# Performance work log

Measured on AMD Instinct MI355X. Metric: run time of the kernel, lower is better.

## Reference

```python
import jax, jax.numpy as jnp
import numpy as np

N = 20000
NEG_SLOPE = 0.2


def gat_conv(x, src, dst, W, att_src, att_dst, bias, heads, ch, concat):
    # x: [N, F_in]; src/dst: [E] (messages flow src -> dst, softmax grouped by dst)
    n = x.shape[0]
    h = (x @ W).reshape(n, heads, ch)                      # [N, H, C]
    a_s = jnp.sum(h * att_src, axis=-1)                    # [N, H]
    a_d = jnp.sum(h * att_dst, axis=-1)                    # [N, H]
    e = jax.nn.leaky_relu(a_s[src] + a_d[dst], NEG_SLOPE)  # [E, H]
    m = jax.ops.segment_max(e, dst, num_segments=n)        # segment-softmax (stable)
    ex = jnp.exp(e - m[dst])
    denom = jax.ops.segment_sum(ex, dst, num_segments=n)
    alpha = ex / (denom[dst] + 1e-16)                      # [E, H]
    msg = h[src] * alpha[:, :, None]                       # [E, H, C]
    out = jax.ops.segment_sum(msg, dst, num_segments=n)    # [N, H, C]
    out = out.reshape(n, heads * ch) if concat else out.mean(axis=1)
    return out + bias


def setup_inputs() -> dict:
    key = jax.random.key(0)
    ks = jax.random.split(key, 24)
    in_ch, h_ch, out_ch, H, OH = 512, 128, 64, 4, 6
    hid = H * h_ch  # 512
    s = 0.1
    d = {
        "x": jax.random.normal(ks[0], (N, in_ch), jnp.float32),
        "edge_index": jax.random.randint(ks[1], (2, 160000), 0, N, jnp.int32),
        "W1": jax.random.normal(ks[2], (in_ch, H * h_ch), jnp.float32) * s,
        "as1": jax.random.normal(ks[3], (1, H, h_ch), jnp.float32) * s,
        "ad1": jax.random.normal(ks[4], (1, H, h_ch), jnp.float32) * s,
        "b1": jnp.zeros((H * h_ch,), jnp.float32),
        "lW1": jax.random.normal(ks[5], (in_ch, hid), jnp.float32) * s,
        "lb1": jnp.zeros((hid,), jnp.float32),
        "W2": jax.random.normal(ks[6], (hid, H * h_ch), jnp.float32) * s,
        "as2": jax.random.normal(ks[7], (1, H, h_ch), jnp.float32) * s,
        "ad2": jax.random.normal(ks[8], (1, H, h_ch), jnp.float32) * s,
        "b2": jnp.zeros((H * h_ch,), jnp.float32),
        "lW2": jax.random.normal(ks[9], (hid, hid), jnp.float32) * s,
        "lb2": jnp.zeros((hid,), jnp.float32),
        "W3": jax.random.normal(ks[10], (hid, OH * out_ch), jnp.float32) * s,
        "as3": jax.random.normal(ks[11], (1, OH, out_ch), jnp.float32) * s,
        "ad3": jax.random.normal(ks[12], (1, OH, out_ch), jnp.float32) * s,
        "b3": jnp.zeros((out_ch,), jnp.float32),
        "lW3": jax.random.normal(ks[13], (hid, out_ch), jnp.float32) * s,
        "lb3": jnp.zeros((out_ch,), jnp.float32),
    }
    return d


def reference(x, edge_index, W1, as1, ad1, b1, lW1, lb1,
              W2, as2, ad2, b2, lW2, lb2,
              W3, as3, ad3, b3, lW3, lb3):
    n = x.shape[0]
    loops = jnp.arange(n, dtype=edge_index.dtype)  # PyG GATConv add_self_loops=True
    src = jnp.concatenate([edge_index[0], loops])
    dst = jnp.concatenate([edge_index[1], loops])
    h = jax.nn.elu(gat_conv(x, src, dst, W1, as1, ad1, b1, 4, 128, True) + x @ lW1 + lb1)
    h = jax.nn.elu(gat_conv(h, src, dst, W2, as2, ad2, b2, 4, 128, True) + h @ lW2 + lb2)
    out = gat_conv(h, src, dst, W3, as3, ad3, b3, 6, 64, False) + h @ lW3 + lb3
    return out
```

## Files before the change

### kernel.cpp

```cpp
#include <hip/hip_runtime.h>
#include <cstddef>
#include <cstdint>
#include <type_traits>

#define N_NODES 20000
#define NPAD 20096
#define E0_EDGES 160000
#define E_TOT (E0_EDGES + N_NODES)
#define CAP 64

typedef __bf16 bf16x8 __attribute__((ext_vector_type(8)));
typedef float f32x4 __attribute__((ext_vector_type(4)));

__device__ __forceinline__ ushort f2bf(float f) {
  uint32_t u = __float_as_uint(f);
  return (ushort)((u + 0x7FFFu + ((u >> 16) & 1u)) >> 16);
}
__device__ __forceinline__ float bf2f(ushort h) {
  return __uint_as_float((uint32_t)h << 16);
}

__device__ __forceinline__ int SW(int r) { return ((r >> 1) & 3) ^ ((r >> 3) & 1); }

#define GLOAD16(g, l)                                                         \
  __builtin_amdgcn_global_load_lds(                                           \
      (const __attribute__((address_space(1))) void*)(uintptr_t)(g),          \
      (__attribute__((address_space(3))) void*)(uint32_t)(uintptr_t)(l),      \
      16, 0, 0)


__global__ void fill_csr_kernel(const int* __restrict__ ei, int* __restrict__ cnt,
                                int* __restrict__ slots) {
  int e = blockIdx.x * blockDim.x + threadIdx.x;
  if (e >= E_TOT) return;
  int src, dst;
  if (e < E0_EDGES) { src = ei[e]; dst = ei[E0_EDGES + e]; }
  else              { src = e - E0_EDGES; dst = src; }
  int pos = atomicAdd(&cnt[dst], 1);
  if (pos < CAP) slots[dst * CAP + pos] = src;
}


__global__ void convert_x_kernel(const float* __restrict__ x, ushort* __restrict__ xb) {
  size_t i = ((size_t)blockIdx.x * blockDim.x + threadIdx.x) * 4;
  if (i >= (size_t)NPAD * 512) return;
  if (i < (size_t)N_NODES * 512) {
    float4 v = *(const float4*)(x + i);
    ushort4 o;
    o.x = f2bf(v.x); o.y = f2bf(v.y); o.z = f2bf(v.z); o.w = f2bf(v.w);
    *(ushort4*)(xb + i) = o;
  } else {
    *(ushort4*)(xb + i) = make_ushort4(0, 0, 0, 0);
  }
}

__global__ void transpose_all_kernel(
    const float* __restrict__ W1, const float* __restrict__ lW1,
    const float* __restrict__ W2, const float* __restrict__ lW2,
    const float* __restrict__ W3, const float* __restrict__ lW3,
    ushort* __restrict__ Bt1, ushort* __restrict__ Bt2, ushort* __restrict__ Bt3) {
  __shared__ float tile[32][33];
  const int K = 512;
  int z = blockIdx.z;
  const float* W; ushort* B; int M;
  switch (z) {
    case 0:  W = W1;  B = Bt1;              M = 512; break;
    case 1:  W = lW1; B = Bt1 + 512 * 512;  M = 512; break;
    case 2:  W = W2;  B = Bt2;              M = 512; break;
    case 3:  W = lW2; B = Bt2 + 512 * 512;  M = 512; break;
    case 4:  W = W3;  B = Bt3;              M = 384; break;
    default: W = lW3; B = Bt3 + 384 * 512;  M = 64;  break;
  }
  int mb = blockIdx.x * 32, kb = blockIdx.y * 32;
  if (mb >= M) return;
  int tx = threadIdx.x, ty = threadIdx.y;
#pragma unroll
  for (int i = 0; i < 32; i += 8)
    tile[ty + i][tx] = W[(size_t)(kb + ty + i) * M + mb + tx];
  __syncthreads();
#pragma unroll
  for (int i = 0; i < 32; i += 8)
    B[(size_t)(mb + ty + i) * K + kb + tx] = f2bf(tile[tx][ty + i]);
}


template <typename Out1T>
__global__ __launch_bounds__(256, 2) void mfma_gemm_kernel(
    const ushort* __restrict__ A,
    const ushort* __restrict__ Bt,
    ushort* __restrict__ out0, int ld0, int split,
    Out1T* __restrict__ out1, int ld1, int Mout1, const float* __restrict__ bias1,
    const float* __restrict__ att_sw, const float* __restrict__ att_dw,
    float* __restrict__ a_sp, float* __restrict__ a_dp,
    int nheads, int headC,
    int NT, int nwg) {
  const int K = 512;
  __shared__ __attribute__((aligned(16))) ushort As[5][128][32];
  __shared__ __attribute__((aligned(16))) ushort Bs[5][128][32];

  int q = nwg >> 3, r = nwg & 7;
  int orig = blockIdx.x;
  int xcd = orig & 7, pos = orig >> 3;
  int wgid = (xcd < r ? xcd * (q + 1) : r * (q + 1) + (xcd - r) * q) + pos;
  int by = wgid / NT, bx = wgid - by * NT;
  int bm = by * 128, bn = bx * 128;

  int tid = threadIdx.x, lane = tid & 63, wave = tid >> 6;
  int wrow = (wave >> 1) * 64, wcol = (wave & 1) * 64;

  size_t K2 = (size_t)K * 2;
  int rofs = lane >> 2;
  int gch = (lane & 3) ^ SW(rofs);
  const char* pA[2];
  const char* pB[2];
  int srow[2];
#pragma unroll
  for (int it = 0; it < 2; ++it) {
    int rr = wave * 32 + it * 16 + rofs;
    srow[it] = wave * 32 + it * 16;
    pA[it] = (const char*)A + (size_t)(bm + rr) * K2 + gch * 16;
    pB[it] = (const char*)Bt + (size_t)(bn + rr) * K2 + gch * 16;
  }

  int fr = lane & 15, hi = lane >> 4;
  int rch = hi ^ SW(fr);

  f32x4 acc[4][4] = {};

  char* AsB = (char*)&As[0][0][0];
  char* BsB = (char*)&Bs[0][0][0];

#pragma unroll
  for (int s = 0; s < 4; ++s) {
#pragma unroll
    for (int it = 0; it < 2; ++it) {
      GLOAD16(pA[it], AsB + s * 8192 + srow[it] * 64);
      GLOAD16(pB[it], BsB + s * 8192 + srow[it] * 64);
    }
#pragma unroll
    for (int it = 0; it < 2; ++it) { pA[it] += 64; pB[it] += 64; }
  }

#pragma unroll
  for (int k = 0; k < 16; ++k) {
    if (k < 13)       asm volatile("s_waitcnt vmcnt(12) lgkmcnt(0)" ::: "memory");
    else if (k == 13) asm volatile("s_waitcnt vmcnt(8) lgkmcnt(0)"  ::: "memory");
    else if (k == 14) asm volatile("s_waitcnt vmcnt(4) lgkmcnt(0)"  ::: "memory");
    else              asm volatile("s_waitcnt vmcnt(0) lgkmcnt(0)"  ::: "memory");
    __builtin_amdgcn_s_barrier();
    asm volatile("" ::: "memory");
    if (k + 4 < 16) {
      int ss = (k + 4) % 5;
#pragma unroll
      for (int it = 0; it < 2; ++it) {
        GLOAD16(pA[it], AsB + ss * 8192 + srow[it] * 64);
        GLOAD16(pB[it], BsB + ss * 8192 + srow[it] * 64);
      }
#pragma unroll
      for (int it = 0; it < 2; ++it) { pA[it] += 64; pB[it] += 64; }
    }
    {
      int sc = k % 5;
      bf16x8 af[4], bf[4];
#pragma unroll
      for (int i = 0; i < 4; ++i)
        af[i] = *(const bf16x8*)&As[sc][wrow + i * 16 + fr][rch * 8];
#pragma unroll
      for (int j = 0; j < 4; ++j)
        bf[j] = *(const bf16x8*)&Bs[sc][wcol + j * 16 + fr][rch * 8];
#pragma unroll
      for (int i = 0; i < 4; ++i)
#pragma unroll
        for (int j = 0; j < 4; ++j)
          acc[i][j] = __builtin_amdgcn_mfma_f32_16x16x32_bf16(af[i], bf[j], acc[i][j], 0, 0, 0);
    }
    asm volatile("" ::: "memory");
  }

  int colg = bn + wcol;
  bool lower = colg < split;
  int g4 = hi << 2;
  int ccol = fr;
#pragma unroll
  for (int i = 0; i < 4; ++i) {
#pragma unroll
    for (int rr = 0; rr < 4; ++rr) {
      int row = bm + wrow + g4 + i * 16 + rr;
      if (row >= N_NODES) continue;
#pragma unroll
      for (int j = 0; j < 4; ++j) {
        int col = colg + j * 16 + ccol;
        float v = acc[i][j][rr];
        if (lower) {
          out0[(size_t)row * ld0 + col] = f2bf(v);
        } else {
          int c1 = col - split;
          if (c1 < Mout1) {
            float b = v + bias1[c1];
            if constexpr (std::is_same<Out1T, ushort>::value)
              out1[(size_t)row * ld1 + c1] = f2bf(b);
            else
              out1[(size_t)row * ld1 + c1] = b;
          }
        }
      }
    }
  }

  if (lower) {
    int hd = colg / headC;
    int cb = colg - hd * headC;
    int half = (cb >> 6) & 1;
    float ws4[4], wd4[4];
#pragma unroll
    for (int j = 0; j < 4; ++j) {
      int cc = hd * headC + cb + j * 16 + ccol;
      ws4[j] = att_sw[cc];
      wd4[j] = att_dw[cc];
    }
#pragma unroll
    for (int i = 0; i < 4; ++i) {
#pragma unroll
      for (int rr = 0; rr < 4; ++rr) {
        float ps = 0.f, pd = 0.f;
#pragma unroll
        for (int j = 0; j < 4; ++j) { ps += acc[i][j][rr] * ws4[j]; pd += acc[i][j][rr] * wd4[j]; }
#pragma unroll
        for (int o = 1; o < 16; o <<= 1) { ps += __shfl_xor(ps, o); pd += __shfl_xor(pd, o); }
        if ((lane & 15) == 0) {
          int row = bm + wrow + g4 + i * 16 + rr;
          if (row < N_NODES) {
            size_t idx = ((size_t)row * nheads + hd) * 2;
            if (headC == 128) {
              a_sp[idx + half] = ps;
              a_dp[idx + half] = pd;
            } else {
              a_sp[idx] = ps;  a_sp[idx + 1] = 0.f;
              a_dp[idx] = pd;  a_dp[idx + 1] = 0.f;
            }
          }
        }
      }
    }
  }
}


template <int H, int C>
__global__ __launch_bounds__(128) void gather12_fused(
    const int* __restrict__ cnt, const int* __restrict__ slots,
    const float* __restrict__ a_sp, const float* __restrict__ a_dp,
    const ushort* __restrict__ hbuf, const float* __restrict__ gat_bias,
    const ushort* __restrict__ skip_in, ushort* __restrict__ outbuf) {
  __shared__ float al[H][CAP];
  __shared__ int srcs[CAP];
  int n = blockIdx.x;
  int t = threadIdx.x, lane = t & 63, w = t >> 6;
  int deg = min(cnt[n], CAP);

  int sj = 0;
  if (lane < deg) sj = slots[n * CAP + lane];
#pragma unroll
  for (int hh = 0; hh < 2; ++hh) {
    int hd = 2 * w + hh;
    float e = -1e30f;
    if (lane < deg) {
      size_t is = ((size_t)sj * H + hd) * 2;
      size_t id = ((size_t)n * H + hd) * 2;
      float v = a_sp[is] + a_sp[is + 1] + a_dp[id] + a_dp[id + 1];
      e = v > 0.f ? v : 0.2f * v;
    }
    float m = e;
#pragma unroll
    for (int o = 32; o > 0; o >>= 1) m = fmaxf(m, __shfl_xor(m, o));
    float ex = (lane < deg) ? expf(e - m) : 0.f;
    float s = ex;
#pragma unroll
    for (int o = 32; o > 0; o >>= 1) s += __shfl_xor(s, o);
    float inv = 1.f / (s + 1e-16f);
    if (lane < deg) al[hd][lane] = ex * inv;
  }
  if (w == 0 && lane < deg) srcs[lane] = sj;
  __syncthreads();

  int f0 = 4 * t, hd = t >> 5;
  float a0 = 0.f, a1 = 0.f, a2 = 0.f, a3 = 0.f;
  for (int j = 0; j < deg; ++j) {
    float a = al[hd][j];
    ushort4 hv = *(const ushort4*)(hbuf + (size_t)srcs[j] * (H * C) + f0);
    a0 += a * bf2f(hv.x);
    a1 += a * bf2f(hv.y);
    a2 += a * bf2f(hv.z);
    a3 += a * bf2f(hv.w);
  }
  ushort4 sk = *(const ushort4*)(skip_in + (size_t)n * (H * C) + f0);
  float o0 = a0 + gat_bias[f0 + 0] + bf2f(sk.x);
  float o1 = a1 + gat_bias[f0 + 1] + bf2f(sk.y);
  float o2 = a2 + gat_bias[f0 + 2] + bf2f(sk.z);
  float o3 = a3 + gat_bias[f0 + 3] + bf2f(sk.w);
  o0 = o0 > 0.f ? o0 : (expf(o0) - 1.f);
  o1 = o1 > 0.f ? o1 : (expf(o1) - 1.f);
  o2 = o2 > 0.f ? o2 : (expf(o2) - 1.f);
  o3 = o3 > 0.f ? o3 : (expf(o3) - 1.f);
  ushort4 ov;
  ov.x = f2bf(o0); ov.y = f2bf(o1); ov.z = f2bf(o2); ov.w = f2bf(o3);
  *(ushort4*)(outbuf + (size_t)n * (H * C) + f0) = ov;
}


__global__ __launch_bounds__(128) void gather3_fused(
    const int* __restrict__ cnt, const int* __restrict__ slots,
    const float* __restrict__ a_sp, const float* __restrict__ a_dp,
    const ushort* __restrict__ hbuf , const float* __restrict__ b3,
    float* __restrict__ out ) {
  __shared__ float al[6][CAP];
  __shared__ int srcs[CAP];
  __shared__ float part[2][64];
  int n = blockIdx.x;
  int t = threadIdx.x, lane = t & 63, w = t >> 6;
  int deg = min(cnt[n], CAP);

  int sj = 0;
  if (lane < deg) sj = slots[n * CAP + lane];
#pragma unroll
  for (int hh = 0; hh < 3; ++hh) {
    int hd = 3 * w + hh;
    float e = -1e30f;
    if (lane < deg) {
      size_t is = ((size_t)sj * 6 + hd) * 2;
      size_t id = ((size_t)n * 6 + hd) * 2;
      float v = a_sp[is] + a_sp[is + 1] + a_dp[id] + a_dp[id + 1];
      e = v > 0.f ? v : 0.2f * v;
    }
    float m = e;
#pragma unroll
    for (int o = 32; o > 0; o >>= 1) m = fmaxf(m, __shfl_xor(m, o));
    float ex = (lane < deg) ? expf(e - m) : 0.f;
    float s = ex;
#pragma unroll
    for (int o = 32; o > 0; o >>= 1) s += __shfl_xor(s, o);
    float inv = (1.f / 6.f) / (s + 1e-16f);
    if (lane < deg) al[hd][lane] = ex * inv;
  }
  if (w == 0 && lane < deg) srcs[lane] = sj;
  __syncthreads();

  int c = t & 63;
  float acc = 0.f;
  for (int j = w; j < deg; j += 2) {
    const ushort* hr = hbuf + (size_t)srcs[j] * 384 + c;
#pragma unroll
    for (int hd = 0; hd < 6; ++hd) acc += al[hd][j] * bf2f(hr[hd * 64]);
  }
  part[w][c] = acc;
  __syncthreads();
  if (t < 64) {
    size_t oi = (size_t)n * 64 + t;
    out[oi] += part[0][t] + part[1][t] + b3[t];
  }
}


extern "C" void kernel_launch(void* const* d_in, const int* in_sizes, int n_in,
                              void* d_out, int out_size, void* d_ws, size_t ws_size,
                              hipStream_t stream) {
  const float* x   = (const float*)d_in[0];
  const int*   ei  = (const int*)d_in[1];
  const float* W1  = (const float*)d_in[2];
  const float* as1 = (const float*)d_in[3];
  const float* ad1 = (const float*)d_in[4];
  const float* b1  = (const float*)d_in[5];
  const float* lW1 = (const float*)d_in[6];
  const float* lb1 = (const float*)d_in[7];
  const float* W2  = (const float*)d_in[8];
  const float* as2 = (const float*)d_in[9];
  const float* ad2 = (const float*)d_in[10];
  const float* b2  = (const float*)d_in[11];
  const float* lW2 = (const float*)d_in[12];
  const float* lb2 = (const float*)d_in[13];
  const float* W3  = (const float*)d_in[14];
  const float* as3 = (const float*)d_in[15];
  const float* ad3 = (const float*)d_in[16];
  const float* b3  = (const float*)d_in[17];
  const float* lW3 = (const float*)d_in[18];
  const float* lb3 = (const float*)d_in[19];
  float* out = (float*)d_out;

  char* ws = (char*)d_ws;
  auto alloc = [&](size_t bytes) -> void* {
    void* p = (void*)ws;
    ws += (bytes + 255) & ~(size_t)255;
    return p;
  };
  ushort* xb    = (ushort*)alloc((size_t)NPAD * 512 * 2);
  ushort* Pb    = (ushort*)alloc((size_t)NPAD * 512 * 2);
  ushort* Qb    = (ushort*)alloc((size_t)NPAD * 512 * 2);
  ushort* skipb = (ushort*)alloc((size_t)N_NODES * 512 * 2);
  ushort* hb    = (ushort*)alloc((size_t)N_NODES * 512 * 2);
  ushort* Bt1   = (ushort*)alloc((size_t)1024 * 512 * 2);
  ushort* Bt2   = (ushort*)alloc((size_t)1024 * 512 * 2);
  ushort* Bt3   = (ushort*)alloc((size_t)512 * 512 * 2);
  float*  a_sp  = (float*)alloc((size_t)N_NODES * 6 * 2 * 4);
  float*  a_dp  = (float*)alloc((size_t)N_NODES * 6 * 2 * 4);
  int*    cnt   = (int*)alloc((size_t)N_NODES * 4);
  int*    slots = (int*)alloc((size_t)N_NODES * CAP * 4);

  hipMemsetAsync(cnt, 0, N_NODES * sizeof(int), stream);
  fill_csr_kernel<<<(E_TOT + 255) / 256, 256, 0, stream>>>(ei, cnt, slots);

  convert_x_kernel<<<((NPAD * 512 / 4) + 255) / 256, 256, 0, stream>>>(x, xb);
  hipMemsetAsync(Pb + (size_t)N_NODES * 512, 0, (size_t)(NPAD - N_NODES) * 512 * 2, stream);
  hipMemsetAsync(Qb + (size_t)N_NODES * 512, 0, (size_t)(NPAD - N_NODES) * 512 * 2, stream);
  transpose_all_kernel<<<dim3(16, 16, 6), dim3(32, 8), 0, stream>>>(
      W1, lW1, W2, lW2, W3, lW3, Bt1, Bt2, Bt3);

  const int NBY = NPAD / 128;
  const int NWG12 = NBY * 8;
  const int NWG3  = NBY * 4;

  mfma_gemm_kernel<ushort><<<NWG12, 256, 0, stream>>>(
      xb, Bt1, hb, 512, 512, skipb, 512, 512, lb1, as1, ad1, a_sp, a_dp, 4, 128,
      8, NWG12);
  gather12_fused<4, 128><<<N_NODES, 128, 0, stream>>>(cnt, slots, a_sp, a_dp, hb, b1, skipb, Pb);

  mfma_gemm_kernel<ushort><<<NWG12, 256, 0, stream>>>(
      Pb, Bt2, hb, 512, 512, skipb, 512, 512, lb2, as2, ad2, a_sp, a_dp, 4, 128,
      8, NWG12);
  gather12_fused<4, 128><<<N_NODES, 128, 0, stream>>>(cnt, slots, a_sp, a_dp, hb, b2, skipb, Qb);

  mfma_gemm_kernel<float><<<NWG3, 256, 0, stream>>>(
      Qb, Bt3, hb, 384, 384, out, 64, 64, lb3, as3, ad3, a_sp, a_dp, 6, 64,
      4, NWG3);
  gather3_fused<<<N_NODES, 128, 0, stream>>>(cnt, slots, a_sp, a_dp, hb, b3, out);
}
```

Baseline: 285.6 us.

## Make MFMA GEMM persistent with 3-stage LDS ring and higher occupancy

The GEMM kernel becomes a persistent grid-stride loop over tiles, capped at 768 workgroups. The LDS ring shrinks from 5 to 3 stages (prefetch depth 4 down to 2) so that 3 workgroups fit per CU, and launch bounds are raised to match. The memsets that zeroed the padding rows of Pb and Qb are removed. The GEMM reads those rows as A inputs (the bm tiles reach NPAD), so they may now hold garbage; those output rows are skipped, so results stay correct as long as the values are finite. Shallower prefetch and tighter register limits trade latency hiding for occupancy.

```diff
diff --git a/kernel.cpp b/kernel.cpp
--- a/kernel.cpp
+++ b/kernel.cpp
@@ -85,7 +85,7 @@
 
 
 template <typename Out1T>
-__global__ __launch_bounds__(256, 2) void mfma_gemm_kernel(
+__global__ __launch_bounds__(256, 3) void mfma_gemm_kernel(
     const ushort* __restrict__ A,
     const ushort* __restrict__ Bt,
     ushort* __restrict__ out0, int ld0, int split,
@@ -95,15 +95,8 @@
     int nheads, int headC,
     int NT, int nwg) {
   const int K = 512;
-  __shared__ __attribute__((aligned(16))) ushort As[5][128][32];
-  __shared__ __attribute__((aligned(16))) ushort Bs[5][128][32];
-
-  int q = nwg >> 3, r = nwg & 7;
-  int orig = blockIdx.x;
-  int xcd = orig & 7, pos = orig >> 3;
-  int wgid = (xcd < r ? xcd * (q + 1) : r * (q + 1) + (xcd - r) * q) + pos;
-  int by = wgid / NT, bx = wgid - by * NT;
-  int bm = by * 128, bn = bx * 128;
+  __shared__ __attribute__((aligned(16))) ushort As[3][128][32];
+  __shared__ __attribute__((aligned(16))) ushort Bs[3][128][32];
 
   int tid = threadIdx.x, lane = tid & 63, wave = tid >> 6;
   int wrow = (wave >> 1) * 64, wcol = (wave & 1) * 64;
@@ -111,132 +104,143 @@
   size_t K2 = (size_t)K * 2;
   int rofs = lane >> 2;
   int gch = (lane & 3) ^ SW(rofs);
-  const char* pA[2];
-  const char* pB[2];
   int srow[2];
 #pragma unroll
-  for (int it = 0; it < 2; ++it) {
-    int rr = wave * 32 + it * 16 + rofs;
-    srow[it] = wave * 32 + it * 16;
-    pA[it] = (const char*)A + (size_t)(bm + rr) * K2 + gch * 16;
-    pB[it] = (const char*)Bt + (size_t)(bn + rr) * K2 + gch * 16;
-  }
+  for (int it = 0; it < 2; ++it) srow[it] = wave * 32 + it * 16;
 
   int fr = lane & 15, hi = lane >> 4;
   int rch = hi ^ SW(fr);
 
-  f32x4 acc[4][4] = {};
-
   char* AsB = (char*)&As[0][0][0];
   char* BsB = (char*)&Bs[0][0][0];
 
-#pragma unroll
-  for (int s = 0; s < 4; ++s) {
+  int q = nwg >> 3, r = nwg & 7;
+
+  for (int w0 = blockIdx.x; w0 < nwg; w0 += gridDim.x) {
+    int xcd = w0 & 7, pos = w0 >> 3;
+    int wgid = (xcd < r ? xcd * (q + 1) : r * (q + 1) + (xcd - r) * q) + pos;
+    int by = wgid / NT, bx = wgid - by * NT;
+    int bm = by * 128, bn = bx * 128;
+
+    const char* pA[2];
+    const char* pB[2];
 #pragma unroll
     for (int it = 0; it < 2; ++it) {
-      GLOAD16(pA[it], AsB + s * 8192 + srow[it] * 64);
-      GLOAD16(pB[it], BsB + s * 8192 + srow[it] * 64);
-    }
-#pragma unroll
-    for (int it = 0; it < 2; ++it) { pA[it] += 64; pB[it] += 64; }
-  }
-
-#pragma unroll
-  for (int k = 0; k < 16; ++k) {
-    if (k < 13)       asm volatile("s_waitcnt vmcnt(12) lgkmcnt(0)" ::: "memory");
-    else if (k == 13) asm volatile("s_waitcnt vmcnt(8) lgkmcnt(0)"  ::: "memory");
-    else if (k == 14) asm volatile("s_waitcnt vmcnt(4) lgkmcnt(0)"  ::: "memory");
-    else              asm volatile("s_waitcnt vmcnt(0) lgkmcnt(0)"  ::: "memory");
+      pA[it] = (const char*)A + (size_t)(bm + srow[it] + rofs) * K2 + gch * 16;
+      pB[it] = (const char*)Bt + (size_t)(bn + srow[it] + rofs) * K2 + gch * 16;
+    }
+
+    f32x4 acc[4][4] = {};
+
+#pragma unroll
+    for (int s = 0; s < 2; ++s) {
+#pragma unroll
+      for (int it = 0; it < 2; ++it) {
+        GLOAD16(pA[it], AsB + s * 8192 + srow[it] * 64);
+        GLOAD16(pB[it], BsB + s * 8192 + srow[it] * 64);
+      }
+#pragma unroll
+      for (int it = 0; it < 2; ++it) { pA[it] += 64; pB[it] += 64; }
+    }
+
+    for (int k = 0; k < 16; ++k) {
+      if (k + 1 < 16) asm volatile("s_waitcnt vmcnt(4) lgkmcnt(0)" ::: "memory");
+      else            asm volatile("s_waitcnt vmcnt(0) lgkmcnt(0)" ::: "memory");
+      __builtin_amdgcn_s_barrier();
+      asm volatile("" ::: "memory");
+      if (k + 2 < 16) {
+        int ss = (k + 2) % 3;
+#pragma unroll
+        for (int it = 0; it < 2; ++it) {
+          GLOAD16(pA[it], AsB + ss * 8192 + srow[it] * 64);
+          GLOAD16(pB[it], BsB + ss * 8192 + srow[it] * 64);
+        }
+#pragma unroll
+        for (int it = 0; it < 2; ++it) { pA[it] += 64; pB[it] += 64; }
+      }
+      {
+        int sc = k % 3;
+        bf16x8 af[4], bf[4];
+#pragma unroll
+        for (int i = 0; i < 4; ++i)
+          af[i] = *(const bf16x8*)&As[sc][wrow + i * 16 + fr][rch * 8];
+#pragma unroll
+        for (int j = 0; j < 4; ++j)
+          bf[j] = *(const bf16x8*)&Bs[sc][wcol + j * 16 + fr][rch * 8];
+#pragma unroll
+        for (int i = 0; i < 4; ++i)
+#pragma unroll
+          for (int j = 0; j < 4; ++j)
+            acc[i][j] = __builtin_amdgcn_mfma_f32_16x16x32_bf16(af[i], bf[j], acc[i][j], 0, 0, 0);
+      }
+      asm volatile("" ::: "memory");
+    }
+
+    asm volatile("s_waitcnt lgkmcnt(0)" ::: "memory");
     __builtin_amdgcn_s_barrier();
     asm volatile("" ::: "memory");
-    if (k + 4 < 16) {
-      int ss = (k + 4) % 5;
-#pragma unroll
-      for (int it = 0; it < 2; ++it) {
-        GLOAD16(pA[it], AsB + ss * 8192 + srow[it] * 64);
-        GLOAD16(pB[it], BsB + ss * 8192 + srow[it] * 64);
-      }
-#pragma unroll
-      for (int it = 0; it < 2; ++it) { pA[it] += 64; pB[it] += 64; }
-    }
-    {
-      int sc = k % 5;
-      bf16x8 af[4], bf[4];
-#pragma unroll
-      for (int i = 0; i < 4; ++i)
-        af[i] = *(const bf16x8*)&As[sc][wrow + i * 16 + fr][rch * 8];
-#pragma unroll
-      for (int j = 0; j < 4; ++j)
-        bf[j] = *(const bf16x8*)&Bs[sc][wcol + j * 16 + fr][rch * 8];
-#pragma unroll
-      for (int i = 0; i < 4; ++i)
-#pragma unroll
-        for (int j = 0; j < 4; ++j)
-          acc[i][j] = __builtin_amdgcn_mfma_f32_16x16x32_bf16(af[i], bf[j], acc[i][j], 0, 0, 0);
-    }
-    asm volatile("" ::: "memory");
-  }
-
-  int colg = bn + wcol;
-  bool lower = colg < split;
-  int g4 = hi << 2;
-  int ccol = fr;
-#pragma unroll
-  for (int i = 0; i < 4; ++i) {
-#pragma unroll
-    for (int rr = 0; rr < 4; ++rr) {
-      int row = bm + wrow + g4 + i * 16 + rr;
-      if (row >= N_NODES) continue;
-#pragma unroll
-      for (int j = 0; j < 4; ++j) {
-        int col = colg + j * 16 + ccol;
-        float v = acc[i][j][rr];
-        if (lower) {
-          out0[(size_t)row * ld0 + col] = f2bf(v);
-        } else {
-          int c1 = col - split;
-          if (c1 < Mout1) {
-            float b = v + bias1[c1];
-            if constexpr (std::is_same<Out1T, ushort>::value)
-              out1[(size_t)row * ld1 + c1] = f2bf(b);
-            else
-              out1[(size_t)row * ld1 + c1] = b;
+
+    int colg = bn + wcol;
+    bool lower = colg < split;
+    int g4 = hi << 2;
+    int ccol = fr;
+#pragma unroll
+    for (int i = 0; i < 4; ++i) {
+#pragma unroll
+      for (int rr = 0; rr < 4; ++rr) {
+        int row = bm + wrow + g4 + i * 16 + rr;
+        if (row >= N_NODES) continue;
+#pragma unroll
+        for (int j = 0; j < 4; ++j) {
+          int col = colg + j * 16 + ccol;
+          float v = acc[i][j][rr];
+          if (lower) {
+            out0[(size_t)row * ld0 + col] = f2bf(v);
+          } else {
+            int c1 = col - split;
+            if (c1 < Mout1) {
+              float b = v + bias1[c1];
+              if constexpr (std::is_same<Out1T, ushort>::value)
+                out1[(size_t)row * ld1 + c1] = f2bf(b);
+              else
+                out1[(size_t)row * ld1 + c1] = b;
+            }
           }
         }
       }
     }
-  }
-
-  if (lower) {
-    int hd = colg / headC;
-    int cb = colg - hd * headC;
-    int half = (cb >> 6) & 1;
-    float ws4[4], wd4[4];
-#pragma unroll
-    for (int j = 0; j < 4; ++j) {
-      int cc = hd * headC + cb + j * 16 + ccol;
-      ws4[j] = att_sw[cc];
-      wd4[j] = att_dw[cc];
-    }
-#pragma unroll
-    for (int i = 0; i < 4; ++i) {
-#pragma unroll
-      for (int rr = 0; rr < 4; ++rr) {
-        float ps = 0.f, pd = 0.f;
-#pragma unroll
-        for (int j = 0; j < 4; ++j) { ps += acc[i][j][rr] * ws4[j]; pd += acc[i][j][rr] * wd4[j]; }
-#pragma unroll
-        for (int o = 1; o < 16; o <<= 1) { ps += __shfl_xor(ps, o); pd += __shfl_xor(pd, o); }
-        if ((lane & 15) == 0) {
-          int row = bm + wrow + g4 + i * 16 + rr;
-          if (row < N_NODES) {
-            size_t idx = ((size_t)row * nheads + hd) * 2;
-            if (headC == 128) {
-              a_sp[idx + half] = ps;
-              a_dp[idx + half] = pd;
-            } else {
-              a_sp[idx] = ps;  a_sp[idx + 1] = 0.f;
-              a_dp[idx] = pd;  a_dp[idx + 1] = 0.f;
+
+    if (lower) {
+      int hd = colg / headC;
+      int cb = colg - hd * headC;
+      int half = (cb >> 6) & 1;
+      float ws4[4], wd4[4];
+#pragma unroll
+      for (int j = 0; j < 4; ++j) {
+        int cc = hd * headC + cb + j * 16 + ccol;
+        ws4[j] = att_sw[cc];
+        wd4[j] = att_dw[cc];
+      }
+#pragma unroll
+      for (int i = 0; i < 4; ++i) {
+#pragma unroll
+        for (int rr = 0; rr < 4; ++rr) {
+          float ps = 0.f, pd = 0.f;
+#pragma unroll
+          for (int j = 0; j < 4; ++j) { ps += acc[i][j][rr] * ws4[j]; pd += acc[i][j][rr] * wd4[j]; }
+#pragma unroll
+          for (int o = 1; o < 16; o <<= 1) { ps += __shfl_xor(ps, o); pd += __shfl_xor(pd, o); }
+          if ((lane & 15) == 0) {
+            int row = bm + wrow + g4 + i * 16 + rr;
+            if (row < N_NODES) {
+              size_t idx = ((size_t)row * nheads + hd) * 2;
+              if (headC == 128) {
+                a_sp[idx + half] = ps;
+                a_dp[idx + half] = pd;
+              } else {
+                a_sp[idx] = ps;  a_sp[idx + 1] = 0.f;
+                a_dp[idx] = pd;  a_dp[idx + 1] = 0.f;
+              }
             }
           }
         }
@@ -409,26 +413,27 @@
   fill_csr_kernel<<<(E_TOT + 255) / 256, 256, 0, stream>>>(ei, cnt, slots);
 
   convert_x_kernel<<<((NPAD * 512 / 4) + 255) / 256, 256, 0, stream>>>(x, xb);
-  hipMemsetAsync(Pb + (size_t)N_NODES * 512, 0, (size_t)(NPAD - N_NODES) * 512 * 2, stream);
-  hipMemsetAsync(Qb + (size_t)N_NODES * 512, 0, (size_t)(NPAD - N_NODES) * 512 * 2, stream);
   transpose_all_kernel<<<dim3(16, 16, 6), dim3(32, 8), 0, stream>>>(
       W1, lW1, W2, lW2, W3, lW3, Bt1, Bt2, Bt3);
 
   const int NBY = NPAD / 128;
   const int NWG12 = NBY * 8;
   const int NWG3  = NBY * 4;
-
-  mfma_gemm_kernel<ushort><<<NWG12, 256, 0, stream>>>(
+  const int PERSIST = 256 * 3;
+  const int G12 = NWG12 < PERSIST ? NWG12 : PERSIST;
+  const int G3  = NWG3  < PERSIST ? NWG3  : PERSIST;
+
+  mfma_gemm_kernel<ushort><<<G12, 256, 0, stream>>>(
       xb, Bt1, hb, 512, 512, skipb, 512, 512, lb1, as1, ad1, a_sp, a_dp, 4, 128,
       8, NWG12);
   gather12_fused<4, 128><<<N_NODES, 128, 0, stream>>>(cnt, slots, a_sp, a_dp, hb, b1, skipb, Pb);
 
-  mfma_gemm_kernel<ushort><<<NWG12, 256, 0, stream>>>(
+  mfma_gemm_kernel<ushort><<<G12, 256, 0, stream>>>(
       Pb, Bt2, hb, 512, 512, skipb, 512, 512, lb2, as2, ad2, a_sp, a_dp, 4, 128,
       8, NWG12);
   gather12_fused<4, 128><<<N_NODES, 128, 0, stream>>>(cnt, slots, a_sp, a_dp, hb, b2, skipb, Qb);
 
-  mfma_gemm_kernel<float><<<NWG3, 256, 0, stream>>>(
+  mfma_gemm_kernel<float><<<G3, 256, 0, stream>>>(
       Qb, Bt3, hb, 384, 384, out, 64, 64, lb3, as3, ad3, a_sp, a_dp, 6, 64,
       4, NWG3);
   gather3_fused<<<N_NODES, 128, 0, stream>>>(cnt, slots, a_sp, a_dp, hb, b3, out);
```

Measured after the change: 259.0 us. 9.3% less time.
